# Performance work log

Measured on AMD Instinct MI355X. Metric: run time of the kernel, lower is better.

The kernel has to match this reference:

```python
import jax, jax.numpy as jnp
import numpy as np

N, E = 50000, 800000
IN_DIM, H_DIM, OUT_DIM, EDGE_DIM, HEADS = 128, 128, 112, 8, 1
NEG_SLOPE = 0.2
BN_EPS = 1e-5


def _gat_layer(x, src, dst, edge_att, W, a_src, a_dst, We, a_edge, bias):
    """PyG GATConv (concat=False, edge_dim used for attention only)."""
    H, C = a_src.shape  # heads, out channels
    xs = (x @ W).reshape(-1, H, C)            # [N,H,C]
    ef = (edge_att @ We).reshape(-1, H, C)    # [E,H,C]
    al_src = jnp.einsum('nhc,hc->nh', xs, a_src)   # [N,H]
    al_dst = jnp.einsum('nhc,hc->nh', xs, a_dst)   # [N,H]
    al_edge = jnp.einsum('ehc,hc->eh', ef, a_edge) # [E,H]
    alpha = al_src[src] + al_dst[dst] + al_edge    # [E,H]
    alpha = jnp.where(alpha > 0, alpha, NEG_SLOPE * alpha)  # leaky_relu(0.2)
    # segment softmax over incoming edges of each dst node
    m = jax.lax.stop_gradient(jax.ops.segment_max(alpha, dst, num_segments=N))
    ex = jnp.exp(alpha - m[dst])
    den = jax.ops.segment_sum(ex, dst, num_segments=N)
    att = ex / den[dst]                       # [E,H]
    msg = xs[src] * att[:, :, None]           # [E,H,C] gather + weight
    out = jax.ops.segment_sum(msg, dst, num_segments=N)  # scatter-add [N,H,C]
    return out.mean(axis=1) + bias            # concat=False -> head mean


def _batchnorm(h, gamma, beta):
    mu = h.mean(axis=0)
    var = h.var(axis=0)
    return gamma * (h - mu) * jax.lax.rsqrt(var + BN_EPS) + beta


def setup_inputs() -> dict:
    key = jax.random.key(0)
    ks = jax.random.split(key, 20)
    s = 0.1
    inp = {
        'x': jax.random.normal(ks[0], (N, IN_DIM), dtype=jnp.float32),
        'edge_index': jax.random.randint(ks[1], (2, E), 0, N, dtype=jnp.int32),
        'edge_att': jax.random.normal(ks[2], (E, EDGE_DIM), dtype=jnp.float32),
        # layer 0: IN_DIM -> H_DIM
        'W0': s * jax.random.normal(ks[3], (IN_DIM, HEADS * H_DIM), dtype=jnp.float32),
        'a_src0': s * jax.random.normal(ks[4], (HEADS, H_DIM), dtype=jnp.float32),
        'a_dst0': s * jax.random.normal(ks[5], (HEADS, H_DIM), dtype=jnp.float32),
        'We0': s * jax.random.normal(ks[6], (EDGE_DIM, HEADS * H_DIM), dtype=jnp.float32),
        'a_edge0': s * jax.random.normal(ks[7], (HEADS, H_DIM), dtype=jnp.float32),
        'b0': jnp.zeros((H_DIM,), dtype=jnp.float32),
        # layer 1: H_DIM -> OUT_DIM
        'W1': s * jax.random.normal(ks[8], (H_DIM, HEADS * OUT_DIM), dtype=jnp.float32),
        'a_src1': s * jax.random.normal(ks[9], (HEADS, OUT_DIM), dtype=jnp.float32),
        'a_dst1': s * jax.random.normal(ks[10], (HEADS, OUT_DIM), dtype=jnp.float32),
        'We1': s * jax.random.normal(ks[11], (EDGE_DIM, HEADS * OUT_DIM), dtype=jnp.float32),
        'a_edge1': s * jax.random.normal(ks[12], (HEADS, OUT_DIM), dtype=jnp.float32),
        'b1': jnp.zeros((OUT_DIM,), dtype=jnp.float32),
        # batchnorms
        'bn_g': jnp.ones((H_DIM,), dtype=jnp.float32),
        'bn_b': jnp.zeros((H_DIM,), dtype=jnp.float32),
        'bnf_g': jnp.ones((OUT_DIM,), dtype=jnp.float32),
        'bnf_b': jnp.zeros((OUT_DIM,), dtype=jnp.float32),
    }
    return inp


def reference(x, edge_index, edge_att,
              W0, a_src0, a_dst0, We0, a_edge0, b0,
              W1, a_src1, a_dst1, We1, a_edge1, b1,
              bn_g, bn_b, bnf_g, bnf_b):
    src, dst = edge_index[0], edge_index[1]
    h = _gat_layer(x, src, dst, edge_att, W0, a_src0, a_dst0, We0, a_edge0, b0)
    h = _batchnorm(h, bn_g, bn_b)
    h = jax.nn.relu(h)
    # dropout is a no-op in eval; omitted for a deterministic reference
    h = _gat_layer(h, src, dst, edge_att, W1, a_src1, a_dst1, We1, a_edge1, b1)
    h = _batchnorm(h, bnf_g, bnf_b)
    return h
```

## Files before the change

### kernel.cpp

```cpp
#include <hip/hip_runtime.h>
#include <math.h>

#define NN 50000
#define NPAD 50048
#define NE 800000
#define SCAN_B 256
#define SCAN_NBLK ((NN + SCAN_B - 1) / SCAN_B)
#define AGG_NBLK 4096

typedef __attribute__((ext_vector_type(8))) short bf16x8;
typedef __attribute__((ext_vector_type(4))) float f32x4;
typedef __attribute__((ext_vector_type(8))) unsigned short u16x8;

__device__ __forceinline__ unsigned short f2bf(float x) {
    unsigned u = __float_as_uint(x);
    u += 0x7fffu + ((u >> 16) & 1);
    return (unsigned short)(u >> 16);
}
__device__ __forceinline__ float bf2f(unsigned short h) {
    return __uint_as_float(((unsigned)h) << 16);
}

__global__ void k_init_cvt(int* __restrict__ deg, float* __restrict__ stats,
                           const float* __restrict__ We0, const float* __restrict__ ae0,
                           const float* __restrict__ We1, const float* __restrict__ ae1,
                           float* __restrict__ ve,
                           const float* __restrict__ W0, const float* __restrict__ W1,
                           unsigned short* __restrict__ Wth0, unsigned short* __restrict__ Wtl0,
                           unsigned short* __restrict__ Wth1, unsigned short* __restrict__ Wtl1)
{
    int idx = blockIdx.x * 256 + threadIdx.x;
    if (idx < NN) deg[idx] = 0;
    if (idx < 512) stats[idx] = 0.f;
    if (idx < 128 * 128) {
        int k = idx / 128, c = idx % 128;
        float v = W0[idx];
        unsigned short hi = f2bf(v);
        Wth0[c * 128 + k] = hi;
        Wtl0[c * 128 + k] = f2bf(v - bf2f(hi));
    } else if (idx < 128 * 128 + 128 * 112) {
        int i2 = idx - 128 * 128;
        int k = i2 / 112, c = i2 % 112;
        float v = W1[i2];
        unsigned short hi = f2bf(v);
        Wth1[c * 128 + k] = hi;
        Wtl1[c * 128 + k] = f2bf(v - bf2f(hi));
    }
    if (blockIdx.x == gridDim.x - 1) {
        int j = threadIdx.x;
        if (j < 8) {
            float s = 0.f;
            for (int c = 0; c < 128; ++c) s += We0[j * 128 + c] * ae0[c];
            ve[j] = s;
        } else if (j < 16) {
            int jj = j - 8;
            float s = 0.f;
            for (int c = 0; c < 112; ++c) s += We1[jj * 112 + c] * ae1[c];
            ve[8 + jj] = s;
        }
    }
}

__global__ void k_deg(const int* __restrict__ dst, int* __restrict__ deg,
                      int* __restrict__ rank, int E_)
{
    int e = blockIdx.x * blockDim.x + threadIdx.x;
    if (e < E_) rank[e] = atomicAdd(&deg[dst[e]], 1);
}

__global__ void k_scan1(const int* __restrict__ deg, int* __restrict__ partial)
{
    __shared__ int sm[SCAN_B];
    int t = threadIdx.x;
    int idx = blockIdx.x * SCAN_B + t;
    sm[t] = (idx < NN) ? deg[idx] : 0;
    __syncthreads();
    #pragma unroll
    for (int off = SCAN_B / 2; off > 0; off >>= 1) {
        if (t < off) sm[t] += sm[t + off];
        __syncthreads();
    }
    if (t == 0) partial[blockIdx.x] = sm[0];
}

__global__ void k_scan3(const int* __restrict__ deg, const int* __restrict__ partial,
                        int* __restrict__ rp)
{
    __shared__ int sm[SCAN_B];
    __shared__ int pbase;
    int t = threadIdx.x;
    int pv = (t < SCAN_NBLK && t < blockIdx.x) ? partial[t] : 0;
    sm[t] = pv;
    __syncthreads();
    #pragma unroll
    for (int off = SCAN_B / 2; off > 0; off >>= 1) {
        if (t < off) sm[t] += sm[t + off];
        __syncthreads();
    }
    if (t == 0) pbase = sm[0];
    __syncthreads();
    int idx = blockIdx.x * SCAN_B + t;
    int v = (idx < NN) ? deg[idx] : 0;
    sm[t] = v;
    __syncthreads();
    #pragma unroll
    for (int off = 1; off < SCAN_B; off <<= 1) {
        int u = (t >= off) ? sm[t - off] : 0;
        __syncthreads();
        sm[t] += u;
        __syncthreads();
    }
    int excl = pbase + ((t == 0) ? 0 : sm[t - 1]);
    if (idx < NN) rp[idx] = excl;
    if (idx == NN - 1) rp[NN] = excl + v;
}

__global__ void k_csr_fill(const int* __restrict__ src, const int* __restrict__ dst,
                           const float* __restrict__ eatt, const float* __restrict__ ve,
                           const int* __restrict__ rp, const int* __restrict__ rank,
                           uint2* __restrict__ pack, int E_)
{
    int e = blockIdx.x * blockDim.x + threadIdx.x;
    if (e >= E_) return;
    const float4* ea = reinterpret_cast<const float4*>(eatt + (size_t)e * 8);
    float4 e0 = ea[0], e1 = ea[1];
    float a0 = e0.x * ve[0] + e0.y * ve[1] + e0.z * ve[2] + e0.w * ve[3]
             + e1.x * ve[4] + e1.y * ve[5] + e1.z * ve[6] + e1.w * ve[7];
    float a1 = e0.x * ve[8] + e0.y * ve[9] + e0.z * ve[10] + e0.w * ve[11]
             + e1.x * ve[12] + e1.y * ve[13] + e1.z * ve[14] + e1.w * ve[15];
    int pos = rp[dst[e]] + rank[e];
    uint2 rec;
    rec.x = (unsigned)src[e];
    rec.y = (unsigned)f2bf(a0) | ((unsigned)f2bf(a1) << 16);
    pack[pos] = rec;
}

template<int COLS, bool BN_IN>
__global__ void k_gemm_mfma(const float* __restrict__ A,
                            const unsigned short* __restrict__ Wth,
                            const unsigned short* __restrict__ Wtl,
                            unsigned short* __restrict__ out,
                            const float* __restrict__ a_src, const float* __restrict__ a_dst,
                            float* __restrict__ als, float* __restrict__ ald,
                            const float* __restrict__ bsum, const float* __restrict__ bsq,
                            const float* __restrict__ gamma, const float* __restrict__ beta)
{
    constexpr int NT = COLS / 16;
    __shared__ float scN[128], shN[128];
    if (BN_IN) {
        if (threadIdx.x < 128) {
            int k = threadIdx.x;
            float invn = 1.0f / (float)NN;
            float mean = bsum[k] * invn;
            float var  = bsq[k] * invn - mean * mean;
            float sc = gamma[k] * rsqrtf(var + 1e-5f);
            scN[k] = sc;
            shN[k] = beta[k] - mean * sc;
        }
        __syncthreads();
    }
    int wv = threadIdx.x >> 6;
    int lane = threadIdx.x & 63;
    int r0 = blockIdx.x * 64 + wv * 16;
    int m = lane & 15;
    int quad = lane >> 4;
    int arow = r0 + m;
    int rc = (arow < NN) ? arow : NN - 1;
    const float* pa = A + (size_t)rc * 128 + quad * 8;

    f32x4 acc[NT];
    #pragma unroll
    for (int t = 0; t < NT; ++t) acc[t] = f32x4{0.f, 0.f, 0.f, 0.f};

    #pragma unroll
    for (int ks = 0; ks < 4; ++ks) {
        float4 v0 = *reinterpret_cast<const float4*>(pa + ks * 32);
        float4 v1 = *reinterpret_cast<const float4*>(pa + ks * 32 + 4);
        float vv[8] = {v0.x, v0.y, v0.z, v0.w, v1.x, v1.y, v1.z, v1.w};
        int kb = ks * 32 + quad * 8;
        bf16x8 ah, al;
        #pragma unroll
        for (int jj = 0; jj < 8; ++jj) {
            float f = vv[jj];
            if (BN_IN) f = fmaxf(f * scN[kb + jj] + shN[kb + jj], 0.f);
            unsigned short hi = f2bf(f);
            ah[jj] = (short)hi;
            al[jj] = (short)f2bf(f - bf2f(hi));
        }
        #pragma unroll
        for (int t = 0; t < NT; ++t) {
            size_t boff = (size_t)(t * 16 + m) * 128 + ks * 32 + quad * 8;
            bf16x8 bh = *reinterpret_cast<const bf16x8*>(Wth + boff);
            bf16x8 bl = *reinterpret_cast<const bf16x8*>(Wtl + boff);
            acc[t] = __builtin_amdgcn_mfma_f32_16x16x32_bf16(ah, bh, acc[t], 0, 0, 0);
            acc[t] = __builtin_amdgcn_mfma_f32_16x16x32_bf16(al, bh, acc[t], 0, 0, 0);
            acc[t] = __builtin_amdgcn_mfma_f32_16x16x32_bf16(ah, bl, acc[t], 0, 0, 0);
        }
    }

    float p[4] = {0.f, 0.f, 0.f, 0.f}, q[4] = {0.f, 0.f, 0.f, 0.f};
    #pragma unroll
    for (int t = 0; t < NT; ++t) {
        int c = t * 16 + m;
        float asv = a_src[c], adv = a_dst[c];
        #pragma unroll
        for (int rI = 0; rI < 4; ++rI) {
            float v = acc[t][rI];
            int row = r0 + quad * 4 + rI;
            if (row < NN) out[(size_t)row * COLS + c] = f2bf(v);
            p[rI] += v * asv;
            q[rI] += v * adv;
        }
    }
    #pragma unroll
    for (int rI = 0; rI < 4; ++rI) {
        #pragma unroll
        for (int off = 1; off <= 8; off <<= 1) {
            p[rI] += __shfl_xor(p[rI], off);
            q[rI] += __shfl_xor(q[rI], off);
        }
    }
    if (m == 0) {
        #pragma unroll
        for (int rI = 0; rI < 4; ++rI) {
            int row = r0 + quad * 4 + rI;
            if (row < NN) { als[row] = p[rI]; ald[row] = q[rI]; }
        }
    }
}

template<int LAYER>
__global__ void k_logit(const int* __restrict__ rp, const uint2* __restrict__ pack,
                        const float* __restrict__ als, const float* __restrict__ ald,
                        uint2* __restrict__ pe)
{
    int wv = threadIdx.x >> 6;
    int lane = threadIdx.x & 63;
    int q = lane >> 4;
    int ql = lane & 15;
    int w = blockIdx.x * 16 + wv * 4 + q;
    if (w >= NN) return;
    int beg = rp[w], end = rp[w + 1];
    float aldv = ald[w];
    for (int p = beg + ql; p < end; p += 16) {
        uint2 r = pack[p];
        float a = als[r.x] + aldv
                + bf2f((unsigned short)(LAYER ? (r.y >> 16) : (r.y & 0xffffu)));
        a = a > 0.f ? a : 0.2f * a;
        uint2 o;
        o.x = r.x;
        o.y = __float_as_uint(__expf(a));
        pe[p] = o;
    }
}

template<int COLS>
__global__ void k_aggregate(const int* __restrict__ rp, const uint2* __restrict__ pe,
                            const unsigned short* __restrict__ xs, float* __restrict__ out,
                            float* __restrict__ psum, float* __restrict__ psq)
{
    __shared__ float sS[4 * 128], sQ[4 * 128];
    int wv = threadIdx.x >> 6;
    int lane = threadIdx.x & 63;
    int q = lane >> 4;
    int ql = lane & 15;
    int col = ql * 8;
    bool act = (col < COLS);
    float bs[8] = {0.f,0.f,0.f,0.f,0.f,0.f,0.f,0.f};
    float bq[8] = {0.f,0.f,0.f,0.f,0.f,0.f,0.f,0.f};

    for (int w = blockIdx.x * 4 + wv; w < NN; w += AGG_NBLK * 4) {
        int beg = rp[w], end = rp[w + 1];
        float acc[8] = {0.f,0.f,0.f,0.f,0.f,0.f,0.f,0.f};
        float den = 0.f;
        int j = beg;
        for (; j + 16 <= end; j += 16) {
            uint2 r0 = pe[j + q];
            uint2 r1 = pe[j + 4 + q];
            uint2 r2 = pe[j + 8 + q];
            uint2 r3 = pe[j + 12 + q];
            float e0 = __uint_as_float(r0.y);
            float e1 = __uint_as_float(r1.y);
            float e2 = __uint_as_float(r2.y);
            float e3 = __uint_as_float(r3.y);
            den += (e0 + e1) + (e2 + e3);
            if (act) {
                u16x8 u0 = *reinterpret_cast<const u16x8*>(xs + (size_t)r0.x * COLS + col);
                u16x8 u1 = *reinterpret_cast<const u16x8*>(xs + (size_t)r1.x * COLS + col);
                u16x8 u2 = *reinterpret_cast<const u16x8*>(xs + (size_t)r2.x * COLS + col);
                u16x8 u3 = *reinterpret_cast<const u16x8*>(xs + (size_t)r3.x * COLS + col);
                #pragma unroll
                for (int k = 0; k < 8; ++k)
                    acc[k] += (e0 * bf2f(u0[k]) + e1 * bf2f(u1[k]))
                            + (e2 * bf2f(u2[k]) + e3 * bf2f(u3[k]));
            }
        }
        if (j < end) {
            int jq = j + q;
            bool v0 = jq      < end;
            bool v1 = jq + 4  < end;
            bool v2 = jq + 8  < end;
            bool v3 = jq + 12 < end;
            uint2 r0 = v0 ? pe[jq]      : uint2{0u, 0u};
            uint2 r1 = v1 ? pe[jq + 4]  : uint2{0u, 0u};
            uint2 r2 = v2 ? pe[jq + 8]  : uint2{0u, 0u};
            uint2 r3 = v3 ? pe[jq + 12] : uint2{0u, 0u};
            float e0 = __uint_as_float(r0.y);
            float e1 = __uint_as_float(r1.y);
            float e2 = __uint_as_float(r2.y);
            float e3 = __uint_as_float(r3.y);
            den += (e0 + e1) + (e2 + e3);
            if (act) {
                u16x8 u0, u1, u2, u3;
                if (v0) u0 = *reinterpret_cast<const u16x8*>(xs + (size_t)r0.x * COLS + col);
                if (v1) u1 = *reinterpret_cast<const u16x8*>(xs + (size_t)r1.x * COLS + col);
                if (v2) u2 = *reinterpret_cast<const u16x8*>(xs + (size_t)r2.x * COLS + col);
                if (v3) u3 = *reinterpret_cast<const u16x8*>(xs + (size_t)r3.x * COLS + col);
                if (v0) {
                    #pragma unroll
                    for (int k = 0; k < 8; ++k) acc[k] += e0 * bf2f(u0[k]);
                }
                if (v1) {
                    #pragma unroll
                    for (int k = 0; k < 8; ++k) acc[k] += e1 * bf2f(u1[k]);
                }
                if (v2) {
                    #pragma unroll
                    for (int k = 0; k < 8; ++k) acc[k] += e2 * bf2f(u2[k]);
                }
                if (v3) {
                    #pragma unroll
                    for (int k = 0; k < 8; ++k) acc[k] += e3 * bf2f(u3[k]);
                }
            }
        }
        #pragma unroll
        for (int k = 0; k < 8; ++k) {
            acc[k] += __shfl_xor(acc[k], 16);
            acc[k] += __shfl_xor(acc[k], 32);
        }
        den += __shfl_xor(den, 16);
        den += __shfl_xor(den, 32);
        float inv = (end > beg) ? 1.f / den : 0.f;
        if (q == 0 && act) {
            float o[8];
            #pragma unroll
            for (int k = 0; k < 8; ++k) {
                o[k] = acc[k] * inv;
                bs[k] += o[k];
                bq[k] += o[k] * o[k];
            }
            f32x4 o0 = {o[0], o[1], o[2], o[3]};
            f32x4 o1 = {o[4], o[5], o[6], o[7]};
            __builtin_nontemporal_store(o0, reinterpret_cast<f32x4*>(out + (size_t)w * COLS + col));
            __builtin_nontemporal_store(o1, reinterpret_cast<f32x4*>(out + (size_t)w * COLS + col + 4));
        }
    }
    if (q == 0) {
        #pragma unroll
        for (int k = 0; k < 8; ++k) {
            sS[wv * 128 + col + k] = bs[k];
            sQ[wv * 128 + col + k] = bq[k];
        }
    }
    __syncthreads();
    int t = threadIdx.x;
    if (t < 128) {
        psum[(size_t)blockIdx.x * 128 + t] = sS[t] + sS[128 + t] + sS[256 + t] + sS[384 + t];
        psq [(size_t)blockIdx.x * 128 + t] = sQ[t] + sQ[128 + t] + sQ[256 + t] + sQ[384 + t];
    }
}

__global__ void k_bn_stats2(const float* __restrict__ psum, const float* __restrict__ psq,
                            float* __restrict__ sums, float* __restrict__ sqs)
{
    int t = threadIdx.x;
    int c = t & 127;
    constexpr int ROWS = AGG_NBLK / 128;
    const float* sp = (t < 128) ? psum : psq;
    float s = 0.f;
    #pragma unroll 4
    for (int i = 0; i < ROWS; ++i)
        s += sp[(size_t)(blockIdx.x * ROWS + i) * 128 + c];
    unsafeAtomicAdd(((t < 128) ? sums : sqs) + c, s);
}

template<int COLS>
__global__ void k_bn_apply(const float* __restrict__ in, float* __restrict__ out,
                           const float* __restrict__ sums, const float* __restrict__ sqs,
                           const float* __restrict__ gamma, const float* __restrict__ beta,
                           int n)
{
    int idx = blockIdx.x * blockDim.x + threadIdx.x;
    if (idx >= n * COLS) return;
    int c = idx % COLS;
    float invn = 1.0f / (float)n;
    float mean = sums[c] * invn;
    float var  = sqs[c] * invn - mean * mean;
    float sc = gamma[c] * rsqrtf(var + 1e-5f);
    float sh = beta[c] - mean * sc;
    out[idx] = in[idx] * sc + sh;
}

extern "C" void kernel_launch(void* const* d_in, const int* in_sizes, int n_in,
                              void* d_out, int out_size, void* d_ws, size_t ws_size,
                              hipStream_t stream)
{
    const float* x    = (const float*)d_in[0];
    const int*   eidx = (const int*)d_in[1];
    const float* eatt = (const float*)d_in[2];
    const float* W0   = (const float*)d_in[3];
    const float* as0  = (const float*)d_in[4];
    const float* ad0  = (const float*)d_in[5];
    const float* We0  = (const float*)d_in[6];
    const float* ae0  = (const float*)d_in[7];
    const float* W1   = (const float*)d_in[9];
    const float* as1  = (const float*)d_in[10];
    const float* ad1  = (const float*)d_in[11];
    const float* We1  = (const float*)d_in[12];
    const float* ae1  = (const float*)d_in[13];
    const float* bng  = (const float*)d_in[15];
    const float* bnb  = (const float*)d_in[16];
    const float* bnfg = (const float*)d_in[17];
    const float* bnfb = (const float*)d_in[18];

    const int N = NN, E = NE;
    const int* src = eidx;
    const int* dst = eidx + E;

    float* ws = (float*)d_ws;
    size_t off = 0;
    unsigned short* xs0b = (unsigned short*)(ws + off); off += (size_t)N * 64;
    float* h   = ws + off;      off += (size_t)N * 128;
    unsigned short* xs1b = (unsigned short*)(ws + off); off += (size_t)N * 56;
    uint2* pack = (uint2*)(ws + off);   off += (size_t)E * 2;
    int*   rp   = (int*)(ws + off);     off += N + 2;
    int*   rank = (int*)(ws + off);     off += E;
    int*   deg  = (int*)(ws + off);     off += N;
    float* als0 = ws + off;     off += N;
    float* ald0 = ws + off;     off += N;
    float* als1 = ws + off;     off += N;
    float* ald1 = ws + off;     off += N;
    float* stats = ws + off;    off += 512;
    float* ve = ws + off;       off += 16;
    int*   partial = (int*)(ws + off);  off += SCAN_NBLK;
    float* psum = ws + off;     off += (size_t)AGG_NBLK * 128;
    float* psq  = ws + off;     off += (size_t)AGG_NBLK * 128;
    unsigned short* Wth0 = (unsigned short*)(ws + off); off += 128 * 64;
    unsigned short* Wtl0 = (unsigned short*)(ws + off); off += 128 * 64;
    unsigned short* Wth1 = (unsigned short*)(ws + off); off += 112 * 64;
    unsigned short* Wtl1 = (unsigned short*)(ws + off); off += 112 * 64;
    float* out1 = h;

    uint2* pe = (uint2*)d_out;

    float* sum0 = stats;
    float* sq0  = stats + 128;
    float* sum1 = stats + 256;
    float* sq1  = stats + 384;

    k_init_cvt<<<(N + 255) / 256, 256, 0, stream>>>(deg, stats, We0, ae0, We1, ae1, ve,
                                                    W0, W1, Wth0, Wtl0, Wth1, Wtl1);

    k_deg<<<(E + 255) / 256, 256, 0, stream>>>(dst, deg, rank, E);
    k_scan1<<<SCAN_NBLK, SCAN_B, 0, stream>>>(deg, partial);
    k_scan3<<<SCAN_NBLK, SCAN_B, 0, stream>>>(deg, partial, rp);
    k_csr_fill<<<(E + 255) / 256, 256, 0, stream>>>(src, dst, eatt, ve, rp, rank, pack, E);

    k_gemm_mfma<128, false><<<NPAD / 64, 256, 0, stream>>>(x, Wth0, Wtl0, xs0b,
                                                           as0, ad0, als0, ald0,
                                                           nullptr, nullptr, nullptr, nullptr);
    k_logit<0><<<(N + 15) / 16, 256, 0, stream>>>(rp, pack, als0, ald0, pe);
    k_aggregate<128><<<AGG_NBLK, 256, 0, stream>>>(rp, pe, xs0b, h, psum, psq);
    k_bn_stats2<<<128, 256, 0, stream>>>(psum, psq, sum0, sq0);

    k_gemm_mfma<112, true><<<NPAD / 64, 256, 0, stream>>>(h, Wth1, Wtl1, xs1b,
                                                          as1, ad1, als1, ald1,
                                                          sum0, sq0, bng, bnb);
    k_logit<1><<<(N + 15) / 16, 256, 0, stream>>>(rp, pack, als1, ald1, pe);
    k_aggregate<112><<<AGG_NBLK, 256, 0, stream>>>(rp, pe, xs1b, out1, psum, psq);
    k_bn_stats2<<<128, 256, 0, stream>>>(psum, psq, sum1, sq1);
    k_bn_apply<112><<<(N * 112 + 255) / 256, 256, 0, stream>>>(out1, (float*)d_out, sum1, sq1, bnfg, bnfb, N);
}
```

Before: 386.4 us.

## Fuse layer-0 logits into CSR fill and give each node a 16-lane group in aggregation

Layer-0 attention logits and their exp are now computed inside the CSR fill kernel, which runs after the first GEMM. This removes the separate layer-0 logit pass and the intermediate pack buffer. The fill writes 16-byte records that hold src, exp0 and the fp32 layer-1 edge logit, and layer 1 reads them through a new logit kernel. Aggregation now gives each destination node one 16-lane group that walks its edges serially, instead of one 64-lane wave split four ways with shuffle reductions, and halves the grid. The costs are wider strided record reads in layer 0, less edge-level parallelism for high-degree nodes, and more shared memory for the BN partial sums.

```diff
diff --git a/kernel.cpp b/kernel.cpp
--- a/kernel.cpp
+++ b/kernel.cpp
@@ -6,7 +6,7 @@
 #define NE 800000
 #define SCAN_B 256
 #define SCAN_NBLK ((NN + SCAN_B - 1) / SCAN_B)
-#define AGG_NBLK 4096
+#define AGG_NBLK 2048
 
 typedef __attribute__((ext_vector_type(8))) short bf16x8;
 typedef __attribute__((ext_vector_type(4))) float f32x4;
@@ -115,10 +115,11 @@
     if (idx == NN - 1) rp[NN] = excl + v;
 }
 
-__global__ void k_csr_fill(const int* __restrict__ src, const int* __restrict__ dst,
-                           const float* __restrict__ eatt, const float* __restrict__ ve,
-                           const int* __restrict__ rp, const int* __restrict__ rank,
-                           uint2* __restrict__ pack, int E_)
+__global__ void k_csr_fill_l0(const int* __restrict__ src, const int* __restrict__ dst,
+                              const float* __restrict__ eatt, const float* __restrict__ ve,
+                              const int* __restrict__ rp, const int* __restrict__ rank,
+                              const float* __restrict__ als, const float* __restrict__ ald,
+                              uint4* __restrict__ pk, int E_)
 {
     int e = blockIdx.x * blockDim.x + threadIdx.x;
     if (e >= E_) return;
@@ -128,11 +129,17 @@
              + e1.x * ve[4] + e1.y * ve[5] + e1.z * ve[6] + e1.w * ve[7];
     float a1 = e0.x * ve[8] + e0.y * ve[9] + e0.z * ve[10] + e0.w * ve[11]
              + e1.x * ve[12] + e1.y * ve[13] + e1.z * ve[14] + e1.w * ve[15];
-    int pos = rp[dst[e]] + rank[e];
-    uint2 rec;
-    rec.x = (unsigned)src[e];
-    rec.y = (unsigned)f2bf(a0) | ((unsigned)f2bf(a1) << 16);
-    pack[pos] = rec;
+    int s = src[e], d = dst[e];
+    float av = als[s] + ald[d] + a0;
+    av = av > 0.f ? av : 0.2f * av;
+    float ex0 = __expf(av);
+    int pos = rp[d] + rank[e];
+    uint4 rec;
+    rec.x = (unsigned)s;
+    rec.y = __float_as_uint(ex0);
+    rec.z = __float_as_uint(a1);
+    rec.w = 0u;
+    pk[pos] = rec;
 }
 
 template<int COLS, bool BN_IN>
@@ -229,23 +236,18 @@
     }
 }
 
-template<int LAYER>
-__global__ void k_logit(const int* __restrict__ rp, const uint2* __restrict__ pack,
-                        const float* __restrict__ als, const float* __restrict__ ald,
-                        uint2* __restrict__ pe)
-{
-    int wv = threadIdx.x >> 6;
-    int lane = threadIdx.x & 63;
-    int q = lane >> 4;
-    int ql = lane & 15;
-    int w = blockIdx.x * 16 + wv * 4 + q;
+__global__ void k_logit1(const int* __restrict__ rp, const uint4* __restrict__ pk,
+                         const float* __restrict__ als, const float* __restrict__ ald,
+                         uint2* __restrict__ pe)
+{
+    int ql = threadIdx.x & 15;
+    int w = blockIdx.x * 16 + (threadIdx.x >> 4);
     if (w >= NN) return;
     int beg = rp[w], end = rp[w + 1];
     float aldv = ald[w];
     for (int p = beg + ql; p < end; p += 16) {
-        uint2 r = pack[p];
-        float a = als[r.x] + aldv
-                + bf2f((unsigned short)(LAYER ? (r.y >> 16) : (r.y & 0xffffu)));
+        uint4 r = pk[p];
+        float a = als[r.x] + aldv + __uint_as_float(r.z);
         a = a > 0.f ? a : 0.2f * a;
         uint2 o;
         o.x = r.x;
@@ -254,31 +256,30 @@
     }
 }
 
-template<int COLS>
+template<int COLS, int RSTRIDE>
 __global__ void k_aggregate(const int* __restrict__ rp, const uint2* __restrict__ pe,
                             const unsigned short* __restrict__ xs, float* __restrict__ out,
                             float* __restrict__ psum, float* __restrict__ psq)
 {
-    __shared__ float sS[4 * 128], sQ[4 * 128];
-    int wv = threadIdx.x >> 6;
-    int lane = threadIdx.x & 63;
-    int q = lane >> 4;
-    int ql = lane & 15;
+    __shared__ float sS[16 * 128], sQ[16 * 128];
+    int ql = threadIdx.x & 15;
+    int wq = threadIdx.x >> 4;
     int col = ql * 8;
     bool act = (col < COLS);
+    int qid = blockIdx.x * 16 + wq;
     float bs[8] = {0.f,0.f,0.f,0.f,0.f,0.f,0.f,0.f};
     float bq[8] = {0.f,0.f,0.f,0.f,0.f,0.f,0.f,0.f};
 
-    for (int w = blockIdx.x * 4 + wv; w < NN; w += AGG_NBLK * 4) {
+    for (int w = qid; w < NN; w += AGG_NBLK * 16) {
         int beg = rp[w], end = rp[w + 1];
         float acc[8] = {0.f,0.f,0.f,0.f,0.f,0.f,0.f,0.f};
         float den = 0.f;
         int j = beg;
-        for (; j + 16 <= end; j += 16) {
-            uint2 r0 = pe[j + q];
-            uint2 r1 = pe[j + 4 + q];
-            uint2 r2 = pe[j + 8 + q];
-            uint2 r3 = pe[j + 12 + q];
+        for (; j + 4 <= end; j += 4) {
+            uint2 r0 = pe[(size_t)(j    ) * RSTRIDE];
+            uint2 r1 = pe[(size_t)(j + 1) * RSTRIDE];
+            uint2 r2 = pe[(size_t)(j + 2) * RSTRIDE];
+            uint2 r3 = pe[(size_t)(j + 3) * RSTRIDE];
             float e0 = __uint_as_float(r0.y);
             float e1 = __uint_as_float(r1.y);
             float e2 = __uint_as_float(r2.y);
@@ -296,53 +297,41 @@
             }
         }
         if (j < end) {
-            int jq = j + q;
-            bool v0 = jq      < end;
-            bool v1 = jq + 4  < end;
-            bool v2 = jq + 8  < end;
-            bool v3 = jq + 12 < end;
-            uint2 r0 = v0 ? pe[jq]      : uint2{0u, 0u};
-            uint2 r1 = v1 ? pe[jq + 4]  : uint2{0u, 0u};
-            uint2 r2 = v2 ? pe[jq + 8]  : uint2{0u, 0u};
-            uint2 r3 = v3 ? pe[jq + 12] : uint2{0u, 0u};
+            bool v1 = j + 1 < end;
+            bool v2 = j + 2 < end;
+            bool v3 = j + 3 < end;
+            uint2 r0 = pe[(size_t)j * RSTRIDE];
+            uint2 r1 = v1 ? pe[(size_t)(j + 1) * RSTRIDE] : uint2{0u, 0u};
+            uint2 r2 = v2 ? pe[(size_t)(j + 2) * RSTRIDE] : uint2{0u, 0u};
+            uint2 r3 = v3 ? pe[(size_t)(j + 3) * RSTRIDE] : uint2{0u, 0u};
             float e0 = __uint_as_float(r0.y);
             float e1 = __uint_as_float(r1.y);
             float e2 = __uint_as_float(r2.y);
             float e3 = __uint_as_float(r3.y);
             den += (e0 + e1) + (e2 + e3);
             if (act) {
-                u16x8 u0, u1, u2, u3;
-                if (v0) u0 = *reinterpret_cast<const u16x8*>(xs + (size_t)r0.x * COLS + col);
-                if (v1) u1 = *reinterpret_cast<const u16x8*>(xs + (size_t)r1.x * COLS + col);
-                if (v2) u2 = *reinterpret_cast<const u16x8*>(xs + (size_t)r2.x * COLS + col);
-                if (v3) u3 = *reinterpret_cast<const u16x8*>(xs + (size_t)r3.x * COLS + col);
-                if (v0) {
-                    #pragma unroll
-                    for (int k = 0; k < 8; ++k) acc[k] += e0 * bf2f(u0[k]);
-                }
+                u16x8 u0 = *reinterpret_cast<const u16x8*>(xs + (size_t)r0.x * COLS + col);
+                #pragma unroll
+                for (int k = 0; k < 8; ++k) acc[k] += e0 * bf2f(u0[k]);
                 if (v1) {
+                    u16x8 u1 = *reinterpret_cast<const u16x8*>(xs + (size_t)r1.x * COLS + col);
                     #pragma unroll
                     for (int k = 0; k < 8; ++k) acc[k] += e1 * bf2f(u1[k]);
                 }
                 if (v2) {
+                    u16x8 u2 = *reinterpret_cast<const u16x8*>(xs + (size_t)r2.x * COLS + col);
                     #pragma unroll
                     for (int k = 0; k < 8; ++k) acc[k] += e2 * bf2f(u2[k]);
                 }
                 if (v3) {
+                    u16x8 u3 = *reinterpret_cast<const u16x8*>(xs + (size_t)r3.x * COLS + col);
                     #pragma unroll
                     for (int k = 0; k < 8; ++k) acc[k] += e3 * bf2f(u3[k]);
                 }
             }
         }
-        #pragma unroll
-        for (int k = 0; k < 8; ++k) {
-            acc[k] += __shfl_xor(acc[k], 16);
-            acc[k] += __shfl_xor(acc[k], 32);
-        }
-        den += __shfl_xor(den, 16);
-        den += __shfl_xor(den, 32);
         float inv = (end > beg) ? 1.f / den : 0.f;
-        if (q == 0 && act) {
+        if (act) {
             float o[8];
             #pragma unroll
             for (int k = 0; k < 8; ++k) {
@@ -356,18 +345,19 @@
             __builtin_nontemporal_store(o1, reinterpret_cast<f32x4*>(out + (size_t)w * COLS + col + 4));
         }
     }
-    if (q == 0) {
-        #pragma unroll
-        for (int k = 0; k < 8; ++k) {
-            sS[wv * 128 + col + k] = bs[k];
-            sQ[wv * 128 + col + k] = bq[k];
-        }
+    #pragma unroll
+    for (int k = 0; k < 8; ++k) {
+        sS[wq * 128 + col + k] = act ? bs[k] : 0.f;
+        sQ[wq * 128 + col + k] = act ? bq[k] : 0.f;
     }
     __syncthreads();
     int t = threadIdx.x;
     if (t < 128) {
-        psum[(size_t)blockIdx.x * 128 + t] = sS[t] + sS[128 + t] + sS[256 + t] + sS[384 + t];
-        psq [(size_t)blockIdx.x * 128 + t] = sQ[t] + sQ[128 + t] + sQ[256 + t] + sQ[384 + t];
+        float s = 0.f, s2 = 0.f;
+        #pragma unroll
+        for (int r = 0; r < 16; ++r) { s += sS[r * 128 + t]; s2 += sQ[r * 128 + t]; }
+        psum[(size_t)blockIdx.x * 128 + t] = s;
+        psq [(size_t)blockIdx.x * 128 + t] = s2;
     }
 }
 
@@ -433,7 +423,6 @@
     unsigned short* xs0b = (unsigned short*)(ws + off); off += (size_t)N * 64;
     float* h   = ws + off;      off += (size_t)N * 128;
     unsigned short* xs1b = (unsigned short*)(ws + off); off += (size_t)N * 56;
-    uint2* pack = (uint2*)(ws + off);   off += (size_t)E * 2;
     int*   rp   = (int*)(ws + off);     off += N + 2;
     int*   rank = (int*)(ws + off);     off += E;
     int*   deg  = (int*)(ws + off);     off += N;
@@ -452,7 +441,8 @@
     unsigned short* Wtl1 = (unsigned short*)(ws + off); off += 112 * 64;
     float* out1 = h;
 
-    uint2* pe = (uint2*)d_out;
+    uint4* pk  = (uint4*)d_out;
+    uint2* pe1 = (uint2*)((char*)d_out + (size_t)E * 16);
 
     float* sum0 = stats;
     float* sq0  = stats + 128;
@@ -465,20 +455,20 @@
     k_deg<<<(E + 255) / 256, 256, 0, stream>>>(dst, deg, rank, E);
     k_scan1<<<SCAN_NBLK, SCAN_B, 0, stream>>>(deg, partial);
     k_scan3<<<SCAN_NBLK, SCAN_B, 0, stream>>>(deg, partial, rp);
-    k_csr_fill<<<(E + 255) / 256, 256, 0, stream>>>(src, dst, eatt, ve, rp, rank, pack, E);
 
     k_gemm_mfma<128, false><<<NPAD / 64, 256, 0, stream>>>(x, Wth0, Wtl0, xs0b,
                                                            as0, ad0, als0, ald0,
                                                            nullptr, nullptr, nullptr, nullptr);
-    k_logit<0><<<(N + 15) / 16, 256, 0, stream>>>(rp, pack, als0, ald0, pe);
-    k_aggregate<128><<<AGG_NBLK, 256, 0, stream>>>(rp, pe, xs0b, h, psum, psq);
+    k_csr_fill_l0<<<(E + 255) / 256, 256, 0, stream>>>(src, dst, eatt, ve, rp, rank,
+                                                       als0, ald0, pk, E);
+    k_aggregate<128, 2><<<AGG_NBLK, 256, 0, stream>>>(rp, (const uint2*)pk, xs0b, h, psum, psq);
     k_bn_stats2<<<128, 256, 0, stream>>>(psum, psq, sum0, sq0);
 
     k_gemm_mfma<112, true><<<NPAD / 64, 256, 0, stream>>>(h, Wth1, Wtl1, xs1b,
                                                           as1, ad1, als1, ald1,
                                                           sum0, sq0, bng, bnb);
-    k_logit<1><<<(N + 15) / 16, 256, 0, stream>>>(rp, pack, als1, ald1, pe);
-    k_aggregate<112><<<AGG_NBLK, 256, 0, stream>>>(rp, pe, xs1b, out1, psum, psq);
+    k_logit1<<<(N + 15) / 16, 256, 0, stream>>>(rp, pk, als1, ald1, pe1);
+    k_aggregate<112, 1><<<AGG_NBLK, 256, 0, stream>>>(rp, pe1, xs1b, out1, psum, psq);
     k_bn_stats2<<<128, 256, 0, stream>>>(psum, psq, sum1, sq1);
     k_bn_apply<112><<<(N * 112 + 255) / 256, 256, 0, stream>>>(out1, (float*)d_out, sum1, sq1, bnfg, bnfb, N);
 }
```

New measurement: 376.1 us. 2.7% less time.
